# Optimization experiments

Measured on AMD Instinct MI355X. Metric: run time of the kernel, lower is better.

The kernel has to match this reference:

```python
import jax, jax.numpy as jnp
import numpy as np

N_NODES = 50000
N_EDGES = 600000
D_FEAT = 128


def setup_inputs() -> dict:
    key = jax.random.key(0)
    k1, k2, k3 = jax.random.split(key, 3)
    x = jax.random.normal(k1, (N_NODES, D_FEAT), dtype=jnp.float32)
    edge_index = jax.random.randint(k2, (2, N_EDGES), 0, N_NODES, dtype=jnp.int64)
    line_graph_val = jax.random.normal(k3, (N_EDGES,), dtype=jnp.float32)  # unused by module
    return {"x": x, "edge_index": edge_index, "line_graph_val": line_graph_val}


def reference(x, edge_index, line_graph_val):
    # edge_index is unpacked as (j, i): j = source, i = target (GCN convention)
    src = edge_index[0]  # j
    dst = edge_index[1]  # i
    n = x.shape[0]
    # deg = scatter-add of ones over target indices i
    deg = jax.ops.segment_sum(jnp.ones_like(src, dtype=x.dtype), dst, num_segments=n)
    # deg^{-1/2}; guard deg==0 (torch would give inf; isolated targets have no edges anyway)
    deg_inv_sqrt = jnp.where(deg > 0, deg ** -0.5, jnp.zeros_like(deg))
    norm = deg_inv_sqrt[src] * deg_inv_sqrt[dst]  # [E]
    # spmm(edge_index[[1,0]], norm, n, n, x): out[i] += norm_e * x[j]
    msg = norm[:, None] * x[src]  # [E, F]
    out = jax.ops.segment_sum(msg, dst, num_segments=n)  # [N, F]
    return jax.nn.relu(out)
```

## Files before the change

kernel.cpp:

```cpp
#include <hip/hip_runtime.h>


#define SORTB    128
#define CHUNKMAX 4704
#define NBP      512
#define BCAP     2048
#define GCAP     512

__device__ __forceinline__ int detect_is64(const unsigned int* w) {
    const int t = threadIdx.x & 63;
    unsigned long long m = __ballot(w[2 * t + 1] != 0u);
    return m == 0ull ? 1 : 0;
}

__device__ __forceinline__ int load_idx(const void* p, long long i, int is64) {
    return is64 ? (int)((const long long*)p)[i] : ((const int*)p)[i];
}

__device__ __forceinline__ unsigned short f2bf(float f) {
    unsigned u = __float_as_uint(f);
    unsigned r = (u + 0x7fffu + ((u >> 16) & 1u)) >> 16;
    return (unsigned short)r;
}

__global__ void k_zero_cur(int* cursor, int nb) {
    for (int i = threadIdx.x; i < nb; i += blockDim.x) cursor[i] = 0;
}

__global__ void __launch_bounds__(256) k_zero(int4* p, int n4) {
    const int stride = gridDim.x * blockDim.x;
    for (int i = blockIdx.x * blockDim.x + threadIdx.x; i < n4; i += stride)
        p[i] = make_int4(0, 0, 0, 0);
}


__global__ void __launch_bounds__(256) k_sort_conv(const void* ei, int* cursor,
                                                   unsigned int* __restrict__ buckets,
                                                   const float* __restrict__ x,
                                                   unsigned short* __restrict__ xb,
                                                   int E, int n, int CH, int nconv) {
    const int bid = blockIdx.x;
    if (bid < SORTB) {
        __shared__ unsigned int raw[CHUNKMAX];
        __shared__ unsigned int srt[CHUNKMAX];
        __shared__ int hist[NBP];
        __shared__ int lbase[NBP];
        __shared__ int gbase[NBP];
        __shared__ int lcur[NBP];
        const int t = threadIdx.x;
        for (int i = t; i < NBP; i += 256) hist[i] = 0;
        __syncthreads();
        const int is64 = detect_is64((const unsigned int*)ei);
        const int e0 = bid * CH;
        const int e1 = min(e0 + CH, E);
        const int nch = e1 - e0;
        for (int i = t; i < nch; i += 256) {
            const long long e = e0 + i;
            int s = load_idx(ei, e, is64);
            int d = load_idx(ei, (long long)E + e, is64);
            unsigned w = ((unsigned)d << 16) | (unsigned)s;
            raw[i] = w;
            atomicAdd(&hist[d >> 7], 1);
        }
        __syncthreads();
        if (t < 64) {
            const int base = t * 8;
            int v[8];
            int sum = 0;
            #pragma unroll
            for (int k = 0; k < 8; ++k) { v[k] = hist[base + k]; sum += v[k]; }
            int pre = sum;
            for (int off = 1; off < 64; off <<= 1) {
                int u = __shfl_up(pre, off);
                if (t >= off) pre += u;
            }
            pre -= sum;
            #pragma unroll
            for (int k = 0; k < 8; ++k) { lbase[base + k] = pre; pre += v[k]; }
        }
        __syncthreads();
        for (int b = t; b < NBP; b += 256) {
            const int c = hist[b];
            gbase[b] = c ? atomicAdd(&cursor[b], c) : 0;
            lcur[b] = lbase[b];
        }
        __syncthreads();
        for (int i = t; i < nch; i += 256) {
            const unsigned w = raw[i];
            const int p = atomicAdd(&lcur[w >> 23], 1);
            srt[p] = w;
        }
        __syncthreads();
        for (int i = t; i < nch; i += 256) {
            const unsigned w = srt[i];
            const int b = w >> 23;
            const int g = gbase[b] + (i - lbase[b]);
            if (g < BCAP) buckets[(size_t)b * BCAP + g] = w;
        }
    } else if (xb) {
        const long long tid = (long long)(bid - SORTB) * 256 + threadIdx.x;
        if (tid < nconv) {
            const long long i = tid * 8;
            float4 a = *(const float4*)(x + i);
            float4 b = *(const float4*)(x + i + 4);
            union { unsigned short us[8]; uint4 v; } o;
            o.us[0] = f2bf(a.x); o.us[1] = f2bf(a.y); o.us[2] = f2bf(a.z); o.us[3] = f2bf(a.w);
            o.us[4] = f2bf(b.x); o.us[5] = f2bf(b.y); o.us[6] = f2bf(b.z); o.us[7] = f2bf(b.w);
            *(uint4*)(xb + i) = o.v;
        }
    }
}

__global__ void __launch_bounds__(128) k_dinv(const int* __restrict__ cursor,
                                              const unsigned int* __restrict__ buckets,
                                              float* __restrict__ dinv, int n) {
    const int b = blockIdx.x;
    __shared__ int h[128];
    const int t = threadIdx.x;
    h[t] = 0;
    __syncthreads();
    const int len = min(cursor[b], BCAP);
    const unsigned int* bb = buckets + (size_t)b * BCAP;
    for (int i = t; i < len; i += 128) atomicAdd(&h[(bb[i] >> 16) & 127], 1);
    __syncthreads();
    const int node = b * 128 + t;
    if (node < n) {
        const int c = h[t];
        dinv[node] = (c > 0) ? rsqrtf((float)c) : 0.f;
    }
}

__global__ void __launch_bounds__(256) k_gather(const unsigned int* __restrict__ buckets,
                                                const int* __restrict__ cursor,
                                                const unsigned short* __restrict__ xb,
                                                const float* __restrict__ dinv,
                                                float* __restrict__ out, int n) {
    const int b = blockIdx.x >> 3;
    const int oct = blockIdx.x & 7;
    __shared__ unsigned int kept[GCAP];
    __shared__ unsigned int srt[GCAP];
    __shared__ int h[16], st[17], lc[16];
    __shared__ int nk;
    const int t = threadIdx.x;
    if (t == 0) nk = 0;
    if (t < 16) h[t] = 0;
    __syncthreads();
    const int len = min(cursor[b], BCAP);
    const unsigned int* bb = buckets + (size_t)b * BCAP;
    for (int i = t; i < len; i += 256) {
        const unsigned w = bb[i];
        const int dl = (w >> 16) & 127;
        if ((dl >> 4) == oct) {
            const int p = atomicAdd(&nk, 1);
            if (p < GCAP) { kept[p] = w; atomicAdd(&h[dl & 15], 1); }
        }
    }
    __syncthreads();
    if (t < 16) {
        const int v = h[t];
        int pre = v;
        for (int off = 1; off < 16; off <<= 1) {
            int u = __shfl_up(pre, off);
            if (t >= off) pre += u;
        }
        pre -= v;
        st[t] = pre; lc[t] = pre;
        if (t == 15) st[16] = pre + v;
    }
    __syncthreads();
    const int nkk = min(nk, GCAP);
    for (int i = t; i < nkk; i += 256) {
        const unsigned w = kept[i];
        const int p = atomicAdd(&lc[(w >> 16) & 15], 1);
        srt[p] = w;
    }
    __syncthreads();
    const int g = t >> 4;
    const int lane = t & 15;
    const int node = b * 128 + oct * 16 + g;
    if (node >= n) return;
    int e = st[g];
    const int eend = st[g + 1];
    float acc[8] = {0.f, 0.f, 0.f, 0.f, 0.f, 0.f, 0.f, 0.f};

    auto accum = [&](int s, float w) {
        uint4 v = ((const uint4*)(xb + (size_t)s * 128))[lane];
        acc[0] += w * __uint_as_float(v.x << 16);
        acc[1] += w * __uint_as_float(v.x & 0xffff0000u);
        acc[2] += w * __uint_as_float(v.y << 16);
        acc[3] += w * __uint_as_float(v.y & 0xffff0000u);
        acc[4] += w * __uint_as_float(v.z << 16);
        acc[5] += w * __uint_as_float(v.z & 0xffff0000u);
        acc[6] += w * __uint_as_float(v.w << 16);
        acc[7] += w * __uint_as_float(v.w & 0xffff0000u);
    };

    for (; e + 3 < eend; e += 4) {
        const int s0 = srt[e] & 0xffff,     s1 = srt[e + 1] & 0xffff;
        const int s2 = srt[e + 2] & 0xffff, s3 = srt[e + 3] & 0xffff;
        const float w0 = dinv[s0], w1 = dinv[s1], w2 = dinv[s2], w3 = dinv[s3];
        accum(s0, w0); accum(s1, w1); accum(s2, w2); accum(s3, w3);
    }
    for (; e < eend; ++e) {
        const int s0 = srt[e] & 0xffff;
        accum(s0, dinv[s0]);
    }
    const float dd = dinv[node];
    float4 o0, o1;
    o0.x = fmaxf(dd * acc[0], 0.f); o0.y = fmaxf(dd * acc[1], 0.f);
    o0.z = fmaxf(dd * acc[2], 0.f); o0.w = fmaxf(dd * acc[3], 0.f);
    o1.x = fmaxf(dd * acc[4], 0.f); o1.y = fmaxf(dd * acc[5], 0.f);
    o1.z = fmaxf(dd * acc[6], 0.f); o1.w = fmaxf(dd * acc[7], 0.f);
    float4* op = (float4*)(out + (size_t)node * 128);
    op[lane * 2] = o0;
    op[lane * 2 + 1] = o1;
}


__global__ void k_fill_direct(const void* ei, int* cnt, int* edges, int E, int cap) {
    const int is64 = detect_is64((const unsigned int*)ei);
    const int stride = gridDim.x * blockDim.x;
    for (int e = blockIdx.x * blockDim.x + threadIdx.x; e < E; e += stride) {
        int s = load_idx(ei, e, is64);
        int d = load_idx(ei, (long long)E + e, is64);
        int pos = atomicAdd(&cnt[d], 1);
        if (pos < cap) edges[(long long)d * cap + pos] = s;
    }
}

__global__ void __launch_bounds__(256) k_gather_pad(const float* __restrict__ x,
                                                    const int* __restrict__ edges,
                                                    const int* __restrict__ cnt,
                                                    float* __restrict__ out, int n, int cap) {
    const int node = blockIdx.x * 8 + (threadIdx.x >> 5);
    if (node >= n) return;
    const int lane = threadIdx.x & 31;
    const int m0 = cnt[node];
    const int m = min(m0, cap);
    const int* eb = edges + (long long)node * cap;
    float ax = 0.f, ay = 0.f, az = 0.f, aw = 0.f;
    int e = 0;
    for (; e + 3 < m; e += 4) {
        int s0 = eb[e], s1 = eb[e + 1], s2 = eb[e + 2], s3 = eb[e + 3];
        int c0 = cnt[s0], c1 = cnt[s1], c2 = cnt[s2], c3 = cnt[s3];
        float4 v0 = *(const float4*)(x + (long long)s0 * 128 + lane * 4);
        float4 v1 = *(const float4*)(x + (long long)s1 * 128 + lane * 4);
        float4 v2 = *(const float4*)(x + (long long)s2 * 128 + lane * 4);
        float4 v3 = *(const float4*)(x + (long long)s3 * 128 + lane * 4);
        float w0 = c0 > 0 ? rsqrtf((float)c0) : 0.f;
        float w1 = c1 > 0 ? rsqrtf((float)c1) : 0.f;
        float w2 = c2 > 0 ? rsqrtf((float)c2) : 0.f;
        float w3 = c3 > 0 ? rsqrtf((float)c3) : 0.f;
        ax += w0 * v0.x + w1 * v1.x + w2 * v2.x + w3 * v3.x;
        ay += w0 * v0.y + w1 * v1.y + w2 * v2.y + w3 * v3.y;
        az += w0 * v0.z + w1 * v1.z + w2 * v2.z + w3 * v3.z;
        aw += w0 * v0.w + w1 * v1.w + w2 * v2.w + w3 * v3.w;
    }
    for (; e < m; ++e) {
        int s0 = eb[e];
        int c0 = cnt[s0];
        float4 v0 = *(const float4*)(x + (long long)s0 * 128 + lane * 4);
        float w0 = c0 > 0 ? rsqrtf((float)c0) : 0.f;
        ax += w0 * v0.x; ay += w0 * v0.y; az += w0 * v0.z; aw += w0 * v0.w;
    }
    const float dd = m0 > 0 ? rsqrtf((float)m0) : 0.f;
    float4 rr;
    rr.x = fmaxf(dd * ax, 0.f); rr.y = fmaxf(dd * ay, 0.f);
    rr.z = fmaxf(dd * az, 0.f); rr.w = fmaxf(dd * aw, 0.f);
    *(float4*)(out + (long long)node * 128 + lane * 4) = rr;
}


__global__ void k_deg_simple(const void* ei, float* deg, int E) {
    const int is64 = detect_is64((const unsigned int*)ei);
    const int stride = gridDim.x * blockDim.x;
    for (int e = blockIdx.x * blockDim.x + threadIdx.x; e < E; e += stride)
        atomicAdd(&deg[load_idx(ei, (long long)E + e, is64)], 1.0f);
}
__global__ void k_dinv_simple(float* deg, int n) {
    int i = blockIdx.x * blockDim.x + threadIdx.x;
    if (i < n) { float d = deg[i]; deg[i] = d > 0.f ? rsqrtf(d) : 0.f; }
}
__global__ void k_scatter_atomic(const float* __restrict__ x, const void* ei,
                                 const float* __restrict__ dinv, float* out, int E) {
    const int is64 = detect_is64((const unsigned int*)ei);
    const int lane = threadIdx.x & 31;
    const int eslot = threadIdx.x >> 5;
    const int stride = gridDim.x * 8;
    for (int e = blockIdx.x * 8 + eslot; e < E; e += stride) {
        int s = load_idx(ei, e, is64);
        int d = load_idx(ei, (long long)E + e, is64);
        float norm = dinv[s] * dinv[d];
        float4 v = ((const float4*)(x + (long long)s * 128))[lane];
        float* o = out + (long long)d * 128 + lane * 4;
        atomicAdd(o + 0, norm * v.x); atomicAdd(o + 1, norm * v.y);
        atomicAdd(o + 2, norm * v.z); atomicAdd(o + 3, norm * v.w);
    }
}
__global__ void k_relu4(float4* out, int n4) {
    const int stride = gridDim.x * blockDim.x;
    for (int i = blockIdx.x * blockDim.x + threadIdx.x; i < n4; i += stride) {
        float4 v = out[i];
        v.x = fmaxf(v.x, 0.f); v.y = fmaxf(v.y, 0.f);
        v.z = fmaxf(v.z, 0.f); v.w = fmaxf(v.w, 0.f);
        out[i] = v;
    }
}

extern "C" void kernel_launch(void* const* d_in, const int* in_sizes, int n_in,
                              void* d_out, int out_size, void* d_ws, size_t ws_size,
                              hipStream_t stream) {
    const float* x = (const float*)d_in[0];
    const void* ei = d_in[1];
    const int D = 128;
    const int n = in_sizes[0] / D;
    const int E = in_sizes[1] / 2;

    char* ws = (char*)d_ws;
    size_t off = 0;
    auto alloc = [&](size_t bytes) {
        char* p = ws + off;
        off += (bytes + 255) & ~(size_t)255;
        return p;
    };
    auto al = [](size_t b) { return (b + 255) & ~(size_t)255; };

    const int nb = (n + 127) / 128;
    const int CH = (E + SORTB - 1) / SORTB;
    const size_t szCur  = al((size_t)nb * 4);
    const size_t szDinv = al((size_t)n * 4);
    const size_t szBkt  = al((size_t)nb * BCAP * 4);
    const size_t szXb   = al((size_t)n * D * 2);
    const size_t needS  = szCur + szDinv + szBkt + szXb;

    if (n <= 65536 && CH <= CHUNKMAX && nb <= NBP && ws_size >= needS) {
        int*   cursor = (int*)alloc(szCur);
        float* dinv   = (float*)alloc(szDinv);
        unsigned int* buckets = (unsigned int*)alloc(szBkt);
        unsigned short* xb    = (unsigned short*)alloc(szXb);

        k_zero_cur<<<1, 512, 0, stream>>>(cursor, nb);
        const int nconv = n * D / 8;
        const int grid1 = SORTB + (nconv + 255) / 256;
        k_sort_conv<<<grid1, 256, 0, stream>>>(ei, cursor, buckets, x, xb, E, n, CH, nconv);
        k_dinv<<<nb, 128, 0, stream>>>(cursor, buckets, dinv, n);
        k_gather<<<nb * 8, 256, 0, stream>>>(buckets, cursor, xb, dinv, (float*)d_out, n);
        return;
    }

    auto needD = [&](int c) { return al((size_t)n * 4) + al((size_t)n * c * 4); };
    if (ws_size >= needD(48)) {
        int c = (ws_size >= needD(64)) ? 64 : 48;
        int* cnt   = (int*)alloc((size_t)n * 4);
        int* edges = (int*)alloc((size_t)n * c * 4);
        k_zero<<<(n / 4 + 255) / 256, 256, 0, stream>>>((int4*)cnt, n / 4);
        k_fill_direct<<<2048, 256, 0, stream>>>(ei, cnt, edges, E, c);
        k_gather_pad<<<(n + 7) / 8, 256, 0, stream>>>(x, edges, cnt, (float*)d_out, n, c);
        return;
    }

    float* deg = (float*)alloc((size_t)n * 4);
    hipMemsetAsync(deg, 0, (size_t)n * sizeof(float), stream);
    hipMemsetAsync(d_out, 0, (size_t)out_size * sizeof(float), stream);
    k_deg_simple<<<2048, 256, 0, stream>>>(ei, deg, E);
    k_dinv_simple<<<(n + 255) / 256, 256, 0, stream>>>(deg, n);
    k_scatter_atomic<<<4096, 256, 0, stream>>>(x, ei, deg, (float*)d_out, E);
    k_relu4<<<2048, 256, 0, stream>>>((float4*)d_out, out_size / 4);
}
```

Baseline: 59.46 us.

## Pre-scale bf16 features by source dinv and fold degree into gather

Splits the fused sort/convert kernel into a standalone sort kernel, now with twice as many blocks and smaller chunks, and a conversion kernel. The conversion kernel computes per-node inverse sqrt degree from the buckets and writes x pre-scaled by it in bf16. This removes the dinv array, the separate k_dinv launch, and the per-edge dinv loads in the gather, which now takes the target degree from the segment length. The gather loop is unrolled to 8 to keep more loads in flight. The cost is that the conversion can no longer overlap with the sort, and each conversion block rescans a bucket to build its histogram.

```diff
diff --git a/kernel.cpp b/kernel.cpp
--- a/kernel.cpp
+++ b/kernel.cpp
@@ -1,8 +1,8 @@
 #include <hip/hip_runtime.h>
 
 
-#define SORTB    128
-#define CHUNKMAX 4704
+#define SORTB    256
+#define CHUNKMAX 2368
 #define NBP      512
 #define BCAP     2048
 #define GCAP     512
@@ -34,106 +34,109 @@
 }
 
 
-__global__ void __launch_bounds__(256) k_sort_conv(const void* ei, int* cursor,
-                                                   unsigned int* __restrict__ buckets,
-                                                   const float* __restrict__ x,
-                                                   unsigned short* __restrict__ xb,
-                                                   int E, int n, int CH, int nconv) {
+__global__ void __launch_bounds__(256) k_sort(const void* ei, int* cursor,
+                                              unsigned int* __restrict__ buckets,
+                                              int E, int CH) {
+    __shared__ unsigned int raw[CHUNKMAX];
+    __shared__ unsigned int srt[CHUNKMAX];
+    __shared__ int hist[NBP];
+    __shared__ int lbase[NBP];
+    __shared__ int gbase[NBP];
+    __shared__ int lcur[NBP];
     const int bid = blockIdx.x;
-    if (bid < SORTB) {
-        __shared__ unsigned int raw[CHUNKMAX];
-        __shared__ unsigned int srt[CHUNKMAX];
-        __shared__ int hist[NBP];
-        __shared__ int lbase[NBP];
-        __shared__ int gbase[NBP];
-        __shared__ int lcur[NBP];
-        const int t = threadIdx.x;
-        for (int i = t; i < NBP; i += 256) hist[i] = 0;
-        __syncthreads();
-        const int is64 = detect_is64((const unsigned int*)ei);
-        const int e0 = bid * CH;
-        const int e1 = min(e0 + CH, E);
-        const int nch = e1 - e0;
-        for (int i = t; i < nch; i += 256) {
-            const long long e = e0 + i;
-            int s = load_idx(ei, e, is64);
-            int d = load_idx(ei, (long long)E + e, is64);
-            unsigned w = ((unsigned)d << 16) | (unsigned)s;
-            raw[i] = w;
-            atomicAdd(&hist[d >> 7], 1);
+    const int t = threadIdx.x;
+    for (int i = t; i < NBP; i += 256) hist[i] = 0;
+    __syncthreads();
+    const int is64 = detect_is64((const unsigned int*)ei);
+    const int e0 = bid * CH;
+    const int e1 = min(e0 + CH, E);
+    const int nch = e1 - e0;
+    for (int i = t; i < nch; i += 256) {
+        const long long e = e0 + i;
+        int s = load_idx(ei, e, is64);
+        int d = load_idx(ei, (long long)E + e, is64);
+        unsigned w = ((unsigned)d << 16) | (unsigned)s;
+        raw[i] = w;
+        atomicAdd(&hist[d >> 7], 1);
+    }
+    __syncthreads();
+    if (t < 64) {
+        const int base = t * 8;
+        int v[8];
+        int sum = 0;
+        #pragma unroll
+        for (int k = 0; k < 8; ++k) { v[k] = hist[base + k]; sum += v[k]; }
+        int pre = sum;
+        for (int off = 1; off < 64; off <<= 1) {
+            int u = __shfl_up(pre, off);
+            if (t >= off) pre += u;
         }
-        __syncthreads();
-        if (t < 64) {
-            const int base = t * 8;
-            int v[8];
-            int sum = 0;
-            #pragma unroll
-            for (int k = 0; k < 8; ++k) { v[k] = hist[base + k]; sum += v[k]; }
-            int pre = sum;
-            for (int off = 1; off < 64; off <<= 1) {
-                int u = __shfl_up(pre, off);
-                if (t >= off) pre += u;
-            }
-            pre -= sum;
-            #pragma unroll
-            for (int k = 0; k < 8; ++k) { lbase[base + k] = pre; pre += v[k]; }
-        }
-        __syncthreads();
-        for (int b = t; b < NBP; b += 256) {
-            const int c = hist[b];
-            gbase[b] = c ? atomicAdd(&cursor[b], c) : 0;
-            lcur[b] = lbase[b];
-        }
-        __syncthreads();
-        for (int i = t; i < nch; i += 256) {
-            const unsigned w = raw[i];
-            const int p = atomicAdd(&lcur[w >> 23], 1);
-            srt[p] = w;
-        }
-        __syncthreads();
-        for (int i = t; i < nch; i += 256) {
-            const unsigned w = srt[i];
-            const int b = w >> 23;
-            const int g = gbase[b] + (i - lbase[b]);
-            if (g < BCAP) buckets[(size_t)b * BCAP + g] = w;
-        }
-    } else if (xb) {
-        const long long tid = (long long)(bid - SORTB) * 256 + threadIdx.x;
-        if (tid < nconv) {
-            const long long i = tid * 8;
-            float4 a = *(const float4*)(x + i);
-            float4 b = *(const float4*)(x + i + 4);
-            union { unsigned short us[8]; uint4 v; } o;
-            o.us[0] = f2bf(a.x); o.us[1] = f2bf(a.y); o.us[2] = f2bf(a.z); o.us[3] = f2bf(a.w);
-            o.us[4] = f2bf(b.x); o.us[5] = f2bf(b.y); o.us[6] = f2bf(b.z); o.us[7] = f2bf(b.w);
-            *(uint4*)(xb + i) = o.v;
-        }
-    }
-}
-
-__global__ void __launch_bounds__(128) k_dinv(const int* __restrict__ cursor,
-                                              const unsigned int* __restrict__ buckets,
-                                              float* __restrict__ dinv, int n) {
-    const int b = blockIdx.x;
-    __shared__ int h[128];
+        pre -= sum;
+        #pragma unroll
+        for (int k = 0; k < 8; ++k) { lbase[base + k] = pre; pre += v[k]; }
+    }
+    __syncthreads();
+    for (int b = t; b < NBP; b += 256) {
+        const int c = hist[b];
+        gbase[b] = c ? atomicAdd(&cursor[b], c) : 0;
+        lcur[b] = lbase[b];
+    }
+    __syncthreads();
+    for (int i = t; i < nch; i += 256) {
+        const unsigned w = raw[i];
+        const int p = atomicAdd(&lcur[w >> 23], 1);
+        srt[p] = w;
+    }
+    __syncthreads();
+    for (int i = t; i < nch; i += 256) {
+        const unsigned w = srt[i];
+        const int b = w >> 23;
+        const int g = gbase[b] + (i - lbase[b]);
+        if (g < BCAP) buckets[(size_t)b * BCAP + g] = w;
+    }
+}
+
+__global__ void __launch_bounds__(256) k_conv(const unsigned int* __restrict__ buckets,
+                                              const int* __restrict__ cursor,
+                                              const float* __restrict__ x,
+                                              unsigned short* __restrict__ xb, int n) {
+    const int k = blockIdx.x;
+    const int b = k >> 3;
+    const int lo16 = (k & 7) * 16;
+    __shared__ int h[16];
+    __shared__ float sdinv[16];
     const int t = threadIdx.x;
-    h[t] = 0;
+    if (t < 16) h[t] = 0;
     __syncthreads();
     const int len = min(cursor[b], BCAP);
     const unsigned int* bb = buckets + (size_t)b * BCAP;
-    for (int i = t; i < len; i += 128) atomicAdd(&h[(bb[i] >> 16) & 127], 1);
-    __syncthreads();
-    const int node = b * 128 + t;
-    if (node < n) {
+    for (int i = t; i < len; i += 256) {
+        const int dl = ((bb[i] >> 16) & 127) - lo16;
+        if ((unsigned)dl < 16u) atomicAdd(&h[dl], 1);
+    }
+    __syncthreads();
+    if (t < 16) {
         const int c = h[t];
-        dinv[node] = (c > 0) ? rsqrtf((float)c) : 0.f;
+        sdinv[t] = (c > 0) ? rsqrtf((float)c) : 0.f;
+    }
+    __syncthreads();
+    const long long base = (long long)k * 2048 + t * 8;
+    if (base < (long long)n * 128) {
+        const float w = sdinv[t >> 4];
+        float4 a = *(const float4*)(x + base);
+        float4 c = *(const float4*)(x + base + 4);
+        union { unsigned short us[8]; uint4 v; } o;
+        o.us[0] = f2bf(w * a.x); o.us[1] = f2bf(w * a.y);
+        o.us[2] = f2bf(w * a.z); o.us[3] = f2bf(w * a.w);
+        o.us[4] = f2bf(w * c.x); o.us[5] = f2bf(w * c.y);
+        o.us[6] = f2bf(w * c.z); o.us[7] = f2bf(w * c.w);
+        *(uint4*)(xb + base) = o.v;
     }
 }
 
 __global__ void __launch_bounds__(256) k_gather(const unsigned int* __restrict__ buckets,
                                                 const int* __restrict__ cursor,
                                                 const unsigned short* __restrict__ xb,
-                                                const float* __restrict__ dinv,
                                                 float* __restrict__ out, int n) {
     const int b = blockIdx.x >> 3;
     const int oct = blockIdx.x & 7;
@@ -181,31 +184,41 @@
     if (node >= n) return;
     int e = st[g];
     const int eend = st[g + 1];
+    const int deg = eend - e;
     float acc[8] = {0.f, 0.f, 0.f, 0.f, 0.f, 0.f, 0.f, 0.f};
 
-    auto accum = [&](int s, float w) {
-        uint4 v = ((const uint4*)(xb + (size_t)s * 128))[lane];
-        acc[0] += w * __uint_as_float(v.x << 16);
-        acc[1] += w * __uint_as_float(v.x & 0xffff0000u);
-        acc[2] += w * __uint_as_float(v.y << 16);
-        acc[3] += w * __uint_as_float(v.y & 0xffff0000u);
-        acc[4] += w * __uint_as_float(v.z << 16);
-        acc[5] += w * __uint_as_float(v.z & 0xffff0000u);
-        acc[6] += w * __uint_as_float(v.w << 16);
-        acc[7] += w * __uint_as_float(v.w & 0xffff0000u);
+    auto addv = [&](uint4 v) {
+        acc[0] += __uint_as_float(v.x << 16);
+        acc[1] += __uint_as_float(v.x & 0xffff0000u);
+        acc[2] += __uint_as_float(v.y << 16);
+        acc[3] += __uint_as_float(v.y & 0xffff0000u);
+        acc[4] += __uint_as_float(v.z << 16);
+        acc[5] += __uint_as_float(v.z & 0xffff0000u);
+        acc[6] += __uint_as_float(v.w << 16);
+        acc[7] += __uint_as_float(v.w & 0xffff0000u);
     };
 
-    for (; e + 3 < eend; e += 4) {
-        const int s0 = srt[e] & 0xffff,     s1 = srt[e + 1] & 0xffff;
-        const int s2 = srt[e + 2] & 0xffff, s3 = srt[e + 3] & 0xffff;
-        const float w0 = dinv[s0], w1 = dinv[s1], w2 = dinv[s2], w3 = dinv[s3];
-        accum(s0, w0); accum(s1, w1); accum(s2, w2); accum(s3, w3);
-    }
-    for (; e < eend; ++e) {
+    for (; e + 7 < eend; e += 8) {
+        int s[8];
+        uint4 v[8];
+        #pragma unroll
+        for (int k = 0; k < 8; ++k) s[k] = srt[e + k] & 0xffff;
+        #pragma unroll
+        for (int k = 0; k < 8; ++k) v[k] = ((const uint4*)(xb + (size_t)s[k] * 128))[lane];
+        #pragma unroll
+        for (int k = 0; k < 8; ++k) addv(v[k]);
+    }
+    for (; e + 1 < eend; e += 2) {
+        const int s0 = srt[e] & 0xffff, s1 = srt[e + 1] & 0xffff;
+        uint4 v0 = ((const uint4*)(xb + (size_t)s0 * 128))[lane];
+        uint4 v1 = ((const uint4*)(xb + (size_t)s1 * 128))[lane];
+        addv(v0); addv(v1);
+    }
+    if (e < eend) {
         const int s0 = srt[e] & 0xffff;
-        accum(s0, dinv[s0]);
-    }
-    const float dd = dinv[node];
+        addv(((const uint4*)(xb + (size_t)s0 * 128))[lane]);
+    }
+    const float dd = (deg > 0) ? rsqrtf((float)deg) : 0.f;
     float4 o0, o1;
     o0.x = fmaxf(dd * acc[0], 0.f); o0.y = fmaxf(dd * acc[1], 0.f);
     o0.z = fmaxf(dd * acc[2], 0.f); o0.w = fmaxf(dd * acc[3], 0.f);
@@ -327,24 +340,21 @@
 
     const int nb = (n + 127) / 128;
     const int CH = (E + SORTB - 1) / SORTB;
-    const size_t szCur  = al((size_t)nb * 4);
-    const size_t szDinv = al((size_t)n * 4);
-    const size_t szBkt  = al((size_t)nb * BCAP * 4);
-    const size_t szXb   = al((size_t)n * D * 2);
-    const size_t needS  = szCur + szDinv + szBkt + szXb;
+    const size_t szCur = al((size_t)nb * 4);
+    const size_t szBkt = al((size_t)nb * BCAP * 4);
+    const size_t szXb  = al((size_t)n * D * 2);
+    const size_t needS = szCur + szBkt + szXb;
 
     if (n <= 65536 && CH <= CHUNKMAX && nb <= NBP && ws_size >= needS) {
-        int*   cursor = (int*)alloc(szCur);
-        float* dinv   = (float*)alloc(szDinv);
+        int* cursor = (int*)alloc(szCur);
         unsigned int* buckets = (unsigned int*)alloc(szBkt);
-        unsigned short* xb    = (unsigned short*)alloc(szXb);
+        unsigned short* xb = (unsigned short*)alloc(szXb);
 
         k_zero_cur<<<1, 512, 0, stream>>>(cursor, nb);
-        const int nconv = n * D / 8;
-        const int grid1 = SORTB + (nconv + 255) / 256;
-        k_sort_conv<<<grid1, 256, 0, stream>>>(ei, cursor, buckets, x, xb, E, n, CH, nconv);
-        k_dinv<<<nb, 128, 0, stream>>>(cursor, buckets, dinv, n);
-        k_gather<<<nb * 8, 256, 0, stream>>>(buckets, cursor, xb, dinv, (float*)d_out, n);
+        k_sort<<<SORTB, 256, 0, stream>>>(ei, cursor, buckets, E, CH);
+        const int ntiles = (n * D + 2047) / 2048;
+        k_conv<<<ntiles, 256, 0, stream>>>(buckets, cursor, x, xb, n);
+        k_gather<<<nb * 8, 256, 0, stream>>>(buckets, cursor, xb, (float*)d_out, n);
         return;
     }
 
```

After: 61.22 us. 3.0% more time.
